# Optimization experiments

Measured on AMD Instinct MI355X. Metric: run time of the kernel, lower is better.

Reference implementation:

```python
import jax, jax.numpy as jnp
import numpy as np

N, OUT, IN = 16384, 2048, 2048

def setup_inputs() -> dict:
    key = jax.random.key(0)
    k1, k2, k3 = jax.random.split(key, 3)
    input_ = jax.random.normal(k1, (N, IN), dtype=jnp.float32)
    # kaiming normal, fan_in mode: std = sqrt(2/fan_in)
    weight = jax.random.normal(k2, (OUT, IN), dtype=jnp.float32) * np.sqrt(2.0 / IN)
    mask = jax.random.randint(k3, (OUT, IN), 0, 2, dtype=jnp.int32)
    return {"input_": input_, "weight": weight, "mask": mask}

def reference(input_, weight, mask):
    # out = x @ (W * mask)^T  -- mask is a fixed binary expander pattern
    masked_w = weight * mask.astype(weight.dtype)  # [OUT, IN]
    return jnp.matmul(input_, masked_w.T)          # [N, OUT]
```

## Files before the change

kernel.cpp:

```cpp
#include <hip/hip_runtime.h>


#define MDIM 16384
#define NDIM 2048
#define KDIM 2048

#define BM 256
#define BN 256
#define GRID_X ((MDIM / BM) * (NDIM / BN))

using f32x4   = __attribute__((ext_vector_type(4))) float;
using bf16x8  = __attribute__((ext_vector_type(8))) __bf16;
using ushort8 = __attribute__((ext_vector_type(8))) unsigned short;

__device__ __forceinline__ unsigned short f2bf(float f) {
  unsigned int u = __builtin_bit_cast(unsigned int, f);
  u = u + 0x7FFFu + ((u >> 16) & 1u);
  return (unsigned short)(u >> 16);
}


__global__ void convert_input_kernel(const float* __restrict__ in,
                                     unsigned short* __restrict__ out) {
  size_t base = ((size_t)blockIdx.x * blockDim.x + threadIdx.x) * 8;
  float4 a = *reinterpret_cast<const float4*>(in + base);
  float4 b = *reinterpret_cast<const float4*>(in + base + 4);
  ushort8 v;
  v[0] = f2bf(a.x); v[1] = f2bf(a.y); v[2] = f2bf(a.z); v[3] = f2bf(a.w);
  v[4] = f2bf(b.x); v[5] = f2bf(b.y); v[6] = f2bf(b.z); v[7] = f2bf(b.w);
  *reinterpret_cast<ushort8*>(out + base) = v;
}

__global__ void convert_weight_kernel(const float* __restrict__ w,
                                      const int* __restrict__ mk,
                                      unsigned short* __restrict__ out) {
  size_t base = ((size_t)blockIdx.x * blockDim.x + threadIdx.x) * 8;
  float4 a = *reinterpret_cast<const float4*>(w + base);
  float4 b = *reinterpret_cast<const float4*>(w + base + 4);
  int4 m0 = *reinterpret_cast<const int4*>(mk + base);
  int4 m1 = *reinterpret_cast<const int4*>(mk + base + 4);
  ushort8 v;
  v[0] = m0.x ? f2bf(a.x) : (unsigned short)0;
  v[1] = m0.y ? f2bf(a.y) : (unsigned short)0;
  v[2] = m0.z ? f2bf(a.z) : (unsigned short)0;
  v[3] = m0.w ? f2bf(a.w) : (unsigned short)0;
  v[4] = m1.x ? f2bf(b.x) : (unsigned short)0;
  v[5] = m1.y ? f2bf(b.y) : (unsigned short)0;
  v[6] = m1.z ? f2bf(b.z) : (unsigned short)0;
  v[7] = m1.w ? f2bf(b.w) : (unsigned short)0;
  *reinterpret_cast<ushort8*>(out + base) = v;
}


__device__ __forceinline__ f32x4 MF(bf16x8 a, bf16x8 b, f32x4 c) {
  return __builtin_amdgcn_mfma_f32_16x16x32_bf16(a, b, c, 0, 0, 0);
}
__device__ __forceinline__ void bar() {
  asm volatile("" ::: "memory");
  __builtin_amdgcn_s_barrier();
  asm volatile("" ::: "memory");
}
#define VMCNT(n) asm volatile("s_waitcnt vmcnt(" #n ")" ::: "memory")

__global__ __launch_bounds__(512, 2) void gemm_pl(
    const unsigned short* __restrict__ Abf,
    const unsigned short* __restrict__ Bbf,
    float* __restrict__ C) {
  __shared__ __attribute__((aligned(16))) unsigned short Asl[4 * 8192];
  __shared__ __attribute__((aligned(16))) unsigned short Bsl[4 * 8192];

  int bid = blockIdx.x;
  int wgs = (bid & 7) * (GRID_X / 8) + (bid >> 3);
  int tm = wgs >> 3;
  int tn = wgs & 7;
  int row0 = tm * BM, col0 = tn * BN;

  int t = threadIdx.x;
  int lane = t & 63, wid = t >> 6;
  int wr = wid >> 2, wc = wid & 3;
  int fr = lane & 15, fq = lane >> 4;

  int p0 = (wid * 2 + 0) * 64 + lane;
  int r0 = p0 >> 2, kc0 = ((p0 & 3) ^ ((r0 >> 1) & 3)) * 8;
  size_t offA0 = (size_t)(row0 + r0) * KDIM + kc0;
  size_t offB0 = (size_t)(col0 + r0) * KDIM + kc0;
  int ldsw0 = (wid * 2 + 0) * 512;

  int kxor = (fq ^ ((fr >> 1) & 3)) * 8;
  int aoff = (wr * 128 + fr) * 32 + kxor;
  int boff = (wc * 64 + fr) * 32 + kxor;

  f32x4 acc[8][4];
#pragma unroll
  for (int m = 0; m < 8; ++m)
#pragma unroll
    for (int n = 0; n < 4; ++n) acc[m][n] = f32x4{0.f, 0.f, 0.f, 0.f};

  bf16x8 afr[8], bfrA[4], bfrB[4];

#define SLOT_A(b, kh) (Asl + ((b) * 2 + (kh)) * 8192)
#define SLOT_B(b, kh) (Bsl + ((b) * 2 + (kh)) * 8192)

#define STG(slot, base, o0, ke) do {                                            \
  __builtin_amdgcn_global_load_lds(                                             \
      (const __attribute__((address_space(1))) void*)((base) + (o0) + (ke)),    \
      (__attribute__((address_space(3))) void*)((slot) + ldsw0), 16, 0, 0);     \
  __builtin_amdgcn_global_load_lds(                                             \
      (const __attribute__((address_space(1))) void*)((base) + (o0) + 32768 +   \
                                                      (ke)),                    \
      (__attribute__((address_space(3))) void*)((slot) + ldsw0 + 512), 16, 0,   \
      0);                                                                       \
} while (0)

#define PHASE(rb, rkh, SETR, SETU, STAGES, WAITS) do {                          \
  STAGES;                                                                       \
  WAITS;                                                                        \
  bar();                                                                        \
  const unsigned short* _rpa = SLOT_A(rb, rkh) + aoff;                          \
  const unsigned short* _rpb = SLOT_B(rb, rkh) + boff;                          \
  _Pragma("unroll")                                                             \
  for (int _n = 0; _n < 4; ++_n)                                                \
    SETR[_n] = *(const bf16x8*)(_rpb + _n * 512);                               \
  __builtin_amdgcn_s_setprio(1);                                                \
  _Pragma("unroll")                                                             \
  for (int _m = 0; _m < 8; ++_m) {                                              \
    _Pragma("unroll")                                                           \
    for (int _n = 0; _n < 4; ++_n)                                              \
      acc[_m][_n] = MF(afr[_m], SETU[_n], acc[_m][_n]);                         \
    afr[_m] = *(const bf16x8*)(_rpa + _m * 512);                                \
  }                                                                             \
  __builtin_amdgcn_s_setprio(0);                                                \
  bar();                                                                        \
} while (0)

  STG(SLOT_A(0, 0), Abf, offA0, 0);
  STG(SLOT_B(0, 0), Bbf, offB0, 0);
  STG(SLOT_A(0, 1), Abf, offA0, 32);
  STG(SLOT_B(0, 1), Bbf, offB0, 32);
  STG(SLOT_A(1, 0), Abf, offA0, 64);
  STG(SLOT_B(1, 0), Bbf, offB0, 64);
  VMCNT(8);
  bar();
  {
    const unsigned short* pa = SLOT_A(0, 0) + aoff;
    const unsigned short* pb = SLOT_B(0, 0) + boff;
#pragma unroll
    for (int m = 0; m < 8; ++m) afr[m] = *(const bf16x8*)(pa + m * 512);
#pragma unroll
    for (int n = 0; n < 4; ++n) bfrA[n] = *(const bf16x8*)(pb + n * 512);
  }

  for (int i = 0; i < 15; ++i) {
    int kb = i * 128;
    PHASE(0, 1, bfrB, bfrA, { STG(SLOT_A(1, 1), Abf, offA0, kb + 96);
                              STG(SLOT_B(1, 1), Bbf, offB0, kb + 96); }, VMCNT(8));
    PHASE(1, 0, bfrA, bfrB, { STG(SLOT_A(0, 0), Abf, offA0, kb + 128);
                              STG(SLOT_B(0, 0), Bbf, offB0, kb + 128); }, VMCNT(8));
    PHASE(1, 1, bfrB, bfrA, { STG(SLOT_A(0, 1), Abf, offA0, kb + 160);
                              STG(SLOT_B(0, 1), Bbf, offB0, kb + 160); }, VMCNT(8));
    PHASE(0, 0, bfrA, bfrB, { STG(SLOT_A(1, 0), Abf, offA0, kb + 192);
                              STG(SLOT_B(1, 0), Bbf, offB0, kb + 192); }, VMCNT(8));
  }
  PHASE(0, 1, bfrB, bfrA, { STG(SLOT_A(1, 1), Abf, offA0, 2016);
                            STG(SLOT_B(1, 1), Bbf, offB0, 2016); }, VMCNT(8));
  PHASE(1, 0, bfrA, bfrB, , VMCNT(4));
  PHASE(1, 1, bfrB, bfrA, , VMCNT(0));
  {
#pragma unroll
    for (int m = 0; m < 8; ++m)
#pragma unroll
      for (int n = 0; n < 4; ++n)
        acc[m][n] = MF(afr[m], bfrB[n], acc[m][n]);
  }

  size_t crow = (size_t)(row0 + wr * 128 + fq * 4);
  int ccol = col0 + wc * 64 + fr;
#pragma unroll
  for (int m = 0; m < 8; ++m)
#pragma unroll
    for (int n = 0; n < 4; ++n) {
      float* cp = C + (crow + m * 16) * NDIM + ccol + n * 16;
#pragma unroll
      for (int e = 0; e < 4; ++e) cp[(size_t)e * NDIM] = acc[m][n][e];
    }
#undef PHASE
#undef STG
#undef SLOT_A
#undef SLOT_B
}


__global__ __launch_bounds__(256) void gemm_fused_fallback(
    const float* __restrict__ Afp,
    const float* __restrict__ Wfp,
    const int* __restrict__ Mk,
    float* __restrict__ C) {
  __shared__ unsigned short As[128 * 32];
  __shared__ unsigned short Bs[128 * 32];
  int bid = blockIdx.x;
  int nwg = (MDIM / 128) * (NDIM / 128);
  int wg = (bid & 7) * (nwg / 8) + (bid >> 3);
  int tm = wg >> 4, tn = wg & 15;
  int row0 = tm * 128, col0 = tn * 128;
  int t = threadIdx.x;
  int lane = t & 63, wv = t >> 6;
  int wr = wv >> 1, wc = wv & 1;
  int fr = lane & 15, fq = lane >> 4;
  f32x4 acc[4][4];
#pragma unroll
  for (int i = 0; i < 4; ++i)
#pragma unroll
    for (int j = 0; j < 4; ++j) acc[i][j] = f32x4{0.f, 0.f, 0.f, 0.f};
  for (int kt = 0; kt < KDIM; kt += 32) {
#pragma unroll
    for (int j = 0; j < 2; ++j) {
      int c = j * 256 + t;
      int r = c >> 2;
      int ko = (c & 3) * 8;
      const float* ga = Afp + (size_t)(row0 + r) * KDIM + kt + ko;
      float4 a0 = *reinterpret_cast<const float4*>(ga);
      float4 a1 = *reinterpret_cast<const float4*>(ga + 4);
      ushort8 va;
      va[0] = f2bf(a0.x); va[1] = f2bf(a0.y); va[2] = f2bf(a0.z); va[3] = f2bf(a0.w);
      va[4] = f2bf(a1.x); va[5] = f2bf(a1.y); va[6] = f2bf(a1.z); va[7] = f2bf(a1.w);
      *reinterpret_cast<ushort8*>(As + (size_t)c * 8) = va;
      const float* gw = Wfp + (size_t)(col0 + r) * KDIM + kt + ko;
      const int* gm = Mk + (size_t)(col0 + r) * KDIM + kt + ko;
      float4 w0 = *reinterpret_cast<const float4*>(gw);
      float4 w1 = *reinterpret_cast<const float4*>(gw + 4);
      int4 m0 = *reinterpret_cast<const int4*>(gm);
      int4 m1 = *reinterpret_cast<const int4*>(gm + 4);
      ushort8 vb;
      vb[0] = m0.x ? f2bf(w0.x) : (unsigned short)0;
      vb[1] = m0.y ? f2bf(w0.y) : (unsigned short)0;
      vb[2] = m0.z ? f2bf(w0.z) : (unsigned short)0;
      vb[3] = m0.w ? f2bf(w0.w) : (unsigned short)0;
      vb[4] = m1.x ? f2bf(w1.x) : (unsigned short)0;
      vb[5] = m1.y ? f2bf(w1.y) : (unsigned short)0;
      vb[6] = m1.z ? f2bf(w1.z) : (unsigned short)0;
      vb[7] = m1.w ? f2bf(w1.w) : (unsigned short)0;
      *reinterpret_cast<ushort8*>(Bs + (size_t)c * 8) = vb;
    }
    __syncthreads();
    bf16x8 af[4], bfr[4];
#pragma unroll
    for (int m2 = 0; m2 < 4; ++m2)
      af[m2] = *reinterpret_cast<const bf16x8*>(As + (wr * 64 + m2 * 16 + fr) * 32 + fq * 8);
#pragma unroll
    for (int n2 = 0; n2 < 4; ++n2)
      bfr[n2] = *reinterpret_cast<const bf16x8*>(Bs + (wc * 64 + n2 * 16 + fr) * 32 + fq * 8);
#pragma unroll
    for (int m2 = 0; m2 < 4; ++m2)
#pragma unroll
      for (int n2 = 0; n2 < 4; ++n2)
        acc[m2][n2] = MF(af[m2], bfr[n2], acc[m2][n2]);
    __syncthreads();
  }
#pragma unroll
  for (int m2 = 0; m2 < 4; ++m2)
#pragma unroll
    for (int n2 = 0; n2 < 4; ++n2) {
      size_t r0 = (size_t)(row0 + wr * 64 + m2 * 16 + fq * 4);
      size_t c0 = (size_t)(col0 + wc * 64 + n2 * 16 + fr);
#pragma unroll
      for (int i = 0; i < 4; ++i) C[(r0 + i) * NDIM + c0] = acc[m2][n2][i];
    }
}


extern "C" void kernel_launch(void* const* d_in, const int* in_sizes, int n_in,
                              void* d_out, int out_size, void* d_ws, size_t ws_size,
                              hipStream_t stream) {
  const float* input  = (const float*)d_in[0];
  const float* weight = (const float*)d_in[1];
  const int*   mask   = (const int*)d_in[2];
  float* out = (float*)d_out;

  const size_t needA = (size_t)MDIM * KDIM * sizeof(unsigned short);
  const size_t needB = (size_t)NDIM * KDIM * sizeof(unsigned short);

  if (ws_size >= needA + needB) {
    unsigned short* Abf = (unsigned short*)d_ws;
    unsigned short* Bbf = (unsigned short*)((char*)d_ws + needA);
    convert_input_kernel<<<(MDIM * (size_t)KDIM / 8) / 256, 256, 0, stream>>>(input, Abf);
    convert_weight_kernel<<<(NDIM * (size_t)KDIM / 8) / 256, 256, 0, stream>>>(weight, mask, Bbf);
    gemm_pl<<<GRID_X, 512, 0, stream>>>(Abf, Bbf, out);
  } else {
    int nwg = (MDIM / 128) * (NDIM / 128);
    gemm_fused_fallback<<<nwg, 256, 0, stream>>>(input, weight, mask, out);
  }
}
```

Measured before the change: 187.4 us.

## Issue LDS fragment reads via inline asm at phase start, drop register double-buffering

```diff
diff --git a/kernel.cpp b/kernel.cpp
--- a/kernel.cpp
+++ b/kernel.cpp
@@ -12,6 +12,8 @@
 using f32x4   = __attribute__((ext_vector_type(4))) float;
 using bf16x8  = __attribute__((ext_vector_type(8))) __bf16;
 using ushort8 = __attribute__((ext_vector_type(8))) unsigned short;
+
+typedef __attribute__((address_space(3))) const unsigned short* lds_cptr_t;
 
 __device__ __forceinline__ unsigned short f2bf(float f) {
   unsigned int u = __builtin_bit_cast(unsigned int, f);
@@ -55,14 +57,11 @@
 __device__ __forceinline__ f32x4 MF(bf16x8 a, bf16x8 b, f32x4 c) {
   return __builtin_amdgcn_mfma_f32_16x16x32_bf16(a, b, c, 0, 0, 0);
 }
-__device__ __forceinline__ void bar() {
-  asm volatile("" ::: "memory");
-  __builtin_amdgcn_s_barrier();
-  asm volatile("" ::: "memory");
-}
 #define VMCNT(n) asm volatile("s_waitcnt vmcnt(" #n ")" ::: "memory")
-
-__global__ __launch_bounds__(512, 2) void gemm_pl(
+#define DSR(dst, p, off)                                                        \
+  asm volatile("ds_read_b128 %0, %1 offset:%2" : "=v"(dst) : "v"(p), "i"(off))
+
+__global__ __launch_bounds__(512, 2) void gemm_asm(
     const unsigned short* __restrict__ Abf,
     const unsigned short* __restrict__ Bbf,
     float* __restrict__ C) {
@@ -80,23 +79,23 @@
   int wr = wid >> 2, wc = wid & 3;
   int fr = lane & 15, fq = lane >> 4;
 
-  int p0 = (wid * 2 + 0) * 64 + lane;
+  int p0 = (wid * 2) * 64 + lane;
   int r0 = p0 >> 2, kc0 = ((p0 & 3) ^ ((r0 >> 1) & 3)) * 8;
   size_t offA0 = (size_t)(row0 + r0) * KDIM + kc0;
   size_t offB0 = (size_t)(col0 + r0) * KDIM + kc0;
-  int ldsw0 = (wid * 2 + 0) * 512;
+  int ldsw0 = (wid * 2) * 512;
 
   int kxor = (fq ^ ((fr >> 1) & 3)) * 8;
   int aoff = (wr * 128 + fr) * 32 + kxor;
   int boff = (wc * 64 + fr) * 32 + kxor;
+  lds_cptr_t aA = ((lds_cptr_t)Asl) + aoff;
+  lds_cptr_t aB = ((lds_cptr_t)Bsl) + boff;
 
   f32x4 acc[8][4];
 #pragma unroll
   for (int m = 0; m < 8; ++m)
 #pragma unroll
     for (int n = 0; n < 4; ++n) acc[m][n] = f32x4{0.f, 0.f, 0.f, 0.f};
-
-  bf16x8 afr[8], bfrA[4], bfrB[4];
 
 #define SLOT_A(b, kh) (Asl + ((b) * 2 + (kh)) * 8192)
 #define SLOT_B(b, kh) (Bsl + ((b) * 2 + (kh)) * 8192)
@@ -112,25 +111,33 @@
       0);                                                                       \
 } while (0)
 
-#define PHASE(rb, rkh, SETR, SETU, STAGES, WAITS) do {                          \
+#define PHASE(b, kh, STAGES, WAITS) do {                                        \
+  bf16x8 _afr[8], _bfr[4];                                                      \
+  DSR(_afr[0], aA, ((b) * 2 + (kh)) * 16384 + 0 * 1024);                        \
+  DSR(_afr[1], aA, ((b) * 2 + (kh)) * 16384 + 1 * 1024);                        \
+  DSR(_afr[2], aA, ((b) * 2 + (kh)) * 16384 + 2 * 1024);                        \
+  DSR(_afr[3], aA, ((b) * 2 + (kh)) * 16384 + 3 * 1024);                        \
+  DSR(_afr[4], aA, ((b) * 2 + (kh)) * 16384 + 4 * 1024);                        \
+  DSR(_afr[5], aA, ((b) * 2 + (kh)) * 16384 + 5 * 1024);                        \
+  DSR(_afr[6], aA, ((b) * 2 + (kh)) * 16384 + 6 * 1024);                        \
+  DSR(_afr[7], aA, ((b) * 2 + (kh)) * 16384 + 7 * 1024);                        \
+  DSR(_bfr[0], aB, ((b) * 2 + (kh)) * 16384 + 0 * 1024);                        \
+  DSR(_bfr[1], aB, ((b) * 2 + (kh)) * 16384 + 1 * 1024);                        \
+  DSR(_bfr[2], aB, ((b) * 2 + (kh)) * 16384 + 2 * 1024);                        \
+  DSR(_bfr[3], aB, ((b) * 2 + (kh)) * 16384 + 3 * 1024);                        \
   STAGES;                                                                       \
   WAITS;                                                                        \
-  bar();                                                                        \
-  const unsigned short* _rpa = SLOT_A(rb, rkh) + aoff;                          \
-  const unsigned short* _rpb = SLOT_B(rb, rkh) + boff;                          \
-  _Pragma("unroll")                                                             \
-  for (int _n = 0; _n < 4; ++_n)                                                \
-    SETR[_n] = *(const bf16x8*)(_rpb + _n * 512);                               \
+  __builtin_amdgcn_s_barrier();                                                 \
+  asm volatile("s_waitcnt lgkmcnt(0)" ::: "memory");                            \
+  __builtin_amdgcn_sched_barrier(0);                                            \
   __builtin_amdgcn_s_setprio(1);                                                \
   _Pragma("unroll")                                                             \
-  for (int _m = 0; _m < 8; ++_m) {                                              \
+  for (int _m = 0; _m < 8; ++_m)                                                \
     _Pragma("unroll")                                                           \
     for (int _n = 0; _n < 4; ++_n)                                              \
-      acc[_m][_n] = MF(afr[_m], SETU[_n], acc[_m][_n]);                         \
-    afr[_m] = *(const bf16x8*)(_rpa + _m * 512);                                \
-  }                                                                             \
+      acc[_m][_n] = MF(_afr[_m], _bfr[_n], acc[_m][_n]);                        \
   __builtin_amdgcn_s_setprio(0);                                                \
-  bar();                                                                        \
+  __builtin_amdgcn_s_barrier();                                                 \
 } while (0)
 
   STG(SLOT_A(0, 0), Abf, offA0, 0);
@@ -140,37 +147,26 @@
   STG(SLOT_A(1, 0), Abf, offA0, 64);
   STG(SLOT_B(1, 0), Bbf, offB0, 64);
   VMCNT(8);
-  bar();
-  {
-    const unsigned short* pa = SLOT_A(0, 0) + aoff;
-    const unsigned short* pb = SLOT_B(0, 0) + boff;
-#pragma unroll
-    for (int m = 0; m < 8; ++m) afr[m] = *(const bf16x8*)(pa + m * 512);
-#pragma unroll
-    for (int n = 0; n < 4; ++n) bfrA[n] = *(const bf16x8*)(pb + n * 512);
-  }
+  __builtin_amdgcn_s_barrier();
 
   for (int i = 0; i < 15; ++i) {
     int kb = i * 128;
-    PHASE(0, 1, bfrB, bfrA, { STG(SLOT_A(1, 1), Abf, offA0, kb + 96);
-                              STG(SLOT_B(1, 1), Bbf, offB0, kb + 96); }, VMCNT(8));
-    PHASE(1, 0, bfrA, bfrB, { STG(SLOT_A(0, 0), Abf, offA0, kb + 128);
-                              STG(SLOT_B(0, 0), Bbf, offB0, kb + 128); }, VMCNT(8));
-    PHASE(1, 1, bfrB, bfrA, { STG(SLOT_A(0, 1), Abf, offA0, kb + 160);
-                              STG(SLOT_B(0, 1), Bbf, offB0, kb + 160); }, VMCNT(8));
-    PHASE(0, 0, bfrA, bfrB, { STG(SLOT_A(1, 0), Abf, offA0, kb + 192);
-                              STG(SLOT_B(1, 0), Bbf, offB0, kb + 192); }, VMCNT(8));
-  }
-  PHASE(0, 1, bfrB, bfrA, { STG(SLOT_A(1, 1), Abf, offA0, 2016);
-                            STG(SLOT_B(1, 1), Bbf, offB0, 2016); }, VMCNT(8));
-  PHASE(1, 0, bfrA, bfrB, , VMCNT(4));
-  PHASE(1, 1, bfrB, bfrA, , VMCNT(0));
+    PHASE(0, 0, { STG(SLOT_A(1, 1), Abf, offA0, kb + 96);
+                  STG(SLOT_B(1, 1), Bbf, offB0, kb + 96); }, VMCNT(8));
+    PHASE(0, 1, { STG(SLOT_A(0, 0), Abf, offA0, kb + 128);
+                  STG(SLOT_B(0, 0), Bbf, offB0, kb + 128); }, VMCNT(8));
+    PHASE(1, 0, { STG(SLOT_A(0, 1), Abf, offA0, kb + 160);
+                  STG(SLOT_B(0, 1), Bbf, offB0, kb + 160); }, VMCNT(8));
+    PHASE(1, 1, { STG(SLOT_A(1, 0), Abf, offA0, kb + 192);
+                  STG(SLOT_B(1, 0), Bbf, offB0, kb + 192); }, VMCNT(8));
+  }
   {
-#pragma unroll
-    for (int m = 0; m < 8; ++m)
-#pragma unroll
-      for (int n = 0; n < 4; ++n)
-        acc[m][n] = MF(afr[m], bfrB[n], acc[m][n]);
+    int kb = (15) * 128;
+    PHASE(0, 0, { STG(SLOT_A(1, 1), Abf, offA0, kb + 96);
+                  STG(SLOT_B(1, 1), Bbf, offB0, kb + 96); }, VMCNT(8));
+    PHASE(0, 1, , VMCNT(4));
+    PHASE(1, 0, , VMCNT(0));
+    PHASE(1, 1, , );
   }
 
   size_t crow = (size_t)(row0 + wr * 128 + fq * 4);
@@ -284,7 +280,7 @@
     unsigned short* Bbf = (unsigned short*)((char*)d_ws + needA);
     convert_input_kernel<<<(MDIM * (size_t)KDIM / 8) / 256, 256, 0, stream>>>(input, Abf);
     convert_weight_kernel<<<(NDIM * (size_t)KDIM / 8) / 256, 256, 0, stream>>>(weight, mask, Bbf);
-    gemm_pl<<<GRID_X, 512, 0, stream>>>(Abf, Bbf, out);
+    gemm_asm<<<GRID_X, 512, 0, stream>>>(Abf, Bbf, out);
   } else {
     int nwg = (MDIM / 128) * (NDIM / 128);
     gemm_fused_fallback<<<nwg, 256, 0, stream>>>(input, weight, mask, out);
```

After: 174.6 us. 1.07x faster.
